# Kernel tuning notes

Hardware: AMD Instinct MI355X
Metric: run time of the kernel (lower is better)

Reference implementation:

```python
import jax, jax.numpy as jnp
import numpy as np

NUM_TIMESTEPS = 8  # num_timesteps default of CSSMDeiT3Block
LN_EPS = 1e-6      # flax nn.LayerNorm default


def _layernorm(x, scale, bias):
    mu = jnp.mean(x, axis=-1, keepdims=True)
    var = jnp.mean(jnp.square(x - mu), axis=-1, keepdims=True)
    return (x - mu) * jax.lax.rsqrt(var + LN_EPS) * scale + bias


def setup_inputs() -> dict:
    key = jax.random.key(0)
    ks = jax.random.split(key, 8)
    B, H, W, C = 32, 14, 14, 768
    HID = 4 * C
    s = lambda fan: np.float32(1.0 / np.sqrt(fan))
    return {
        "x": jax.random.normal(ks[0], (B, H, W, C), jnp.float32),
        # norm1
        "ln1_scale": jnp.ones((C,), jnp.float32),
        "ln1_bias": jnp.zeros((C,), jnp.float32),
        # GatedCSSM (opponent, concat_xy=True, sigmoid gate)
        "W_in": jax.random.normal(ks[1], (C, C), jnp.float32) * s(C),
        "b_in": jnp.zeros((C,), jnp.float32),
        "W_gate": jax.random.normal(ks[2], (2 * C, C), jnp.float32) * s(2 * C),
        "b_gate": jnp.zeros((C,), jnp.float32),
        "a_decay": jax.random.uniform(ks[3], (C,), jnp.float32, 0.5, 0.99),
        "b_rot": jax.random.normal(ks[4], (C,), jnp.float32) * 0.1,
        "W_out": jax.random.normal(ks[5], (C, C), jnp.float32) * s(C),
        "b_out": jnp.zeros((C,), jnp.float32),
        # layer scales (init_values = 1e-6)
        "gamma1": jnp.full((C,), 1e-6, jnp.float32),
        # norm2 + MLP
        "ln2_scale": jnp.ones((C,), jnp.float32),
        "ln2_bias": jnp.zeros((C,), jnp.float32),
        "W1": jax.random.normal(ks[6], (C, HID), jnp.float32) * s(C),
        "b1": jnp.zeros((HID,), jnp.float32),
        "W2": jax.random.normal(ks[7], (HID, C), jnp.float32) * s(HID),
        "b2": jnp.zeros((C,), jnp.float32),
        "gamma2": jnp.full((C,), 1e-6, jnp.float32),
    }


def reference(x, ln1_scale, ln1_bias, W_in, b_in, W_gate, b_gate, a_decay,
              b_rot, W_out, b_out, gamma1, ln2_scale, ln2_bias,
              W1, b1, W2, b2, gamma2):
    # ---- branch 1: pre-norm -> GatedCSSM (temporal recurrence) -> layerscale -> residual
    residual = x
    xn = _layernorm(x, ln1_scale, ln1_bias)
    # input is repeated over T timesteps, so project once and reuse
    u = xn @ W_in + b_in                       # (B,H,W,C)
    z0 = jnp.zeros_like(u)

    def step(carry, _):
        hx, hy = carry
        # concat_xy=True: gate computed from both opponent states
        g = jax.nn.sigmoid(jnp.concatenate([hx, hy], axis=-1) @ W_gate + b_gate)
        # opponent (rotation/decay) state-space update, gated
        hx_n = g * (a_decay * hx - b_rot * hy) + u
        hy_n = g * (b_rot * hx + a_decay * hy)
        return (hx_n, hy_n), None

    (hx, _hy), _ = jax.lax.scan(step, (z0, z0), None, length=NUM_TIMESTEPS)
    y = hx @ W_out + b_out                     # last-timestep readout (B,H,W,C)
    x = residual + y * gamma1                  # DropPath is identity (rate 0, deterministic)

    # ---- branch 2: pre-norm -> MLP(gelu) -> layerscale -> residual
    residual = x
    xn = _layernorm(x, ln2_scale, ln2_bias)
    h = jax.nn.gelu(xn @ W1 + b1)
    m = h @ W2 + b2
    return residual + m * gamma2
```

## Files before the change

kernel.cpp:

```cpp
#include <hip/hip_runtime.h>
#include <math.h>

typedef __bf16 bf16x8 __attribute__((ext_vector_type(8)));
typedef float  f32x4  __attribute__((ext_vector_type(4)));

#define NROWS 6272
#define CDIM  768
#define HIDD  3072

#define EPI_BIAS 0
#define EPI_GELU 2
#define EPI_RES  3

__device__ __forceinline__ void gload16(const void* g, void* l) {
    __builtin_amdgcn_global_load_lds(
        (const __attribute__((address_space(1))) void*)(uintptr_t)g,
        (__attribute__((address_space(3))) void*)(uintptr_t)l,
        16, 0, 0);
}

__device__ __forceinline__ void xcd_swz(int& m, int& n) {
    const int gx = gridDim.x;
    const int nwg = gx * gridDim.y;
    const int orig = blockIdx.x + gx * blockIdx.y;
    const int q = nwg >> 3, r = nwg & 7;
    const int xcd = orig & 7, loc = orig >> 3;
    const int wg = (xcd < r ? xcd * (q + 1) : r * (q + 1) + (xcd - r) * q) + loc;
    m = wg / gx;
    n = wg % gx;
}

template <int BM, int BN>
__device__ __forceinline__ void gemm_core(const __bf16* __restrict__ A, int lda,
                                          const __bf16* __restrict__ BT, int K,
                                          int m0, int n0,
                                          __bf16* As, __bf16* Bs,
                                          f32x4 acc[BM / 32][BN / 32]) {
    constexpr int RF = BM / 32;
    constexpr int CF = BN / 32;
    const int t  = threadIdx.x;
    const int w  = t >> 6;
    const int l  = t & 63;
    const int wm = w >> 1, wn = w & 1;
    const int rsub = t >> 2;
    const int ke   = (t & 3) * 8;
    const int fr = l & 15;
    const int kq = (l >> 4) * 8;

    const __bf16* gA = A  + (size_t)(m0 + rsub) * lda + ke;
    const __bf16* gB = BT + (size_t)(n0 + rsub) * K   + ke;
    __bf16* lA = &As[w * 512];
    __bf16* lB = &Bs[w * 512];

    for (int k0 = 0; k0 < K; k0 += 32) {
        __syncthreads();
        #pragma unroll
        for (int h = 0; h < BM / 64; ++h)
            gload16(gA + (size_t)(h * 64) * lda + k0, lA + h * 2048);
        #pragma unroll
        for (int h = 0; h < BN / 64; ++h)
            gload16(gB + (size_t)(h * 64) * K + k0, lB + h * 2048);
        __syncthreads();

        bf16x8 av[RF], bv[CF];
        #pragma unroll
        for (int i = 0; i < RF; ++i)
            av[i] = *(const bf16x8*)&As[(wm * (BM / 2) + i * 16 + fr) * 32 + kq];
        #pragma unroll
        for (int j = 0; j < CF; ++j)
            bv[j] = *(const bf16x8*)&Bs[(wn * (BN / 2) + j * 16 + fr) * 32 + kq];
        #pragma unroll
        for (int i = 0; i < RF; ++i)
            #pragma unroll
            for (int j = 0; j < CF; ++j)
                acc[i][j] = __builtin_amdgcn_mfma_f32_16x16x32_bf16(av[i], bv[j], acc[i][j], 0, 0, 0);
    }
}

__global__ __launch_bounds__(256) void transpose_all(const float* __restrict__ W_in,
                                                     const float* __restrict__ W_gate,
                                                     const float* __restrict__ W_out,
                                                     const float* __restrict__ W1,
                                                     const float* __restrict__ W2,
                                                     __bf16* __restrict__ WT_in,
                                                     __bf16* __restrict__ WT_gate,
                                                     __bf16* __restrict__ WT_out,
                                                     __bf16* __restrict__ WT1,
                                                     __bf16* __restrict__ WT2) {
    const int bid = blockIdx.x;
    const float* W; __bf16* WT; int K, N, gx, local;
    if (bid < 576)        { W = W_in;   WT = WT_in;   K = 768;  N = 768;  gx = 24; local = bid; }
    else if (bid < 1728)  { W = W_gate; WT = WT_gate; K = 1536; N = 768;  gx = 24; local = bid - 576; }
    else if (bid < 2304)  { W = W_out;  WT = WT_out;  K = 768;  N = 768;  gx = 24; local = bid - 1728; }
    else if (bid < 4608)  { W = W1;     WT = WT1;     K = 768;  N = 3072; gx = 96; local = bid - 2304; }
    else                  { W = W2;     WT = WT2;     K = 3072; N = 768;  gx = 24; local = bid - 4608; }
    const int nb = (local % gx) * 32;
    const int kb = (local / gx) * 32;

    __shared__ float tile[32][33];
    const int tx = threadIdx.x, ty = threadIdx.y;
    #pragma unroll
    for (int r = 0; r < 4; ++r)
        tile[ty + r * 8][tx] = W[(size_t)(kb + ty + r * 8) * N + nb + tx];
    __syncthreads();
    #pragma unroll
    for (int r = 0; r < 4; ++r)
        WT[(size_t)(nb + ty + r * 8) * K + kb + tx] = (__bf16)tile[tx][ty + r * 8];
}

__global__ __launch_bounds__(256) void ln_kernel(const float* __restrict__ x,
                                                 const float* __restrict__ sc,
                                                 const float* __restrict__ bi,
                                                 __bf16* __restrict__ o) {
    const int row = blockIdx.x;
    const float* xr = x + (size_t)row * CDIM;
    __bf16* orow = o + (size_t)row * CDIM;
    const int t = threadIdx.x;

    float v0 = xr[t], v1 = xr[t + 256], v2 = xr[t + 512];
    float s = v0 + v1 + v2;

    __shared__ float sm[8];
    #pragma unroll
    for (int off = 32; off > 0; off >>= 1) s += __shfl_xor(s, off);
    const int wid = t >> 6, lane = t & 63;
    if (lane == 0) sm[wid] = s;
    __syncthreads();
    const float mu = (sm[0] + sm[1] + sm[2] + sm[3]) * (1.0f / 768.0f);

    const float d0 = v0 - mu, d1 = v1 - mu, d2 = v2 - mu;
    float s2 = d0 * d0 + d1 * d1 + d2 * d2;
    #pragma unroll
    for (int off = 32; off > 0; off >>= 1) s2 += __shfl_xor(s2, off);
    if (lane == 0) sm[4 + wid] = s2;
    __syncthreads();
    const float var = (sm[4] + sm[5] + sm[6] + sm[7]) * (1.0f / 768.0f);
    const float r = rsqrtf(var + 1e-6f);

    orow[t]       = (__bf16)(d0 * r * sc[t]       + bi[t]);
    orow[t + 256] = (__bf16)(d1 * r * sc[t + 256] + bi[t + 256]);
    orow[t + 512] = (__bf16)(d2 * r * sc[t + 512] + bi[t + 512]);
}

template <int EPI, int BM, int BN>
__global__ __launch_bounds__(256) void mm_bf16(const __bf16* __restrict__ A, int lda,
                                               const __bf16* __restrict__ BT,
                                               const float* __restrict__ bias,
                                               const float* __restrict__ gamma,
                                               const float* __restrict__ res, int ldr,
                                               void* __restrict__ outv, int ldo,
                                               int K) {
    constexpr int RF = BM / 32;
    constexpr int CF = BN / 32;
    __shared__ __bf16 As[BM * 32];
    __shared__ __bf16 Bs[BN * 32];
    int mb, nb;
    xcd_swz(mb, nb);
    const int m0 = mb * BM, n0 = nb * BN;

    f32x4 acc[RF][CF];
    #pragma unroll
    for (int i = 0; i < RF; ++i)
        #pragma unroll
        for (int j = 0; j < CF; ++j)
            acc[i][j] = f32x4{0.f, 0.f, 0.f, 0.f};

    gemm_core<BM, BN>(A, lda, BT, K, m0, n0, As, Bs, acc);

    const int l = threadIdx.x & 63;
    const int w = threadIdx.x >> 6;
    const int wm = w >> 1, wn = w & 1;
    const int fr = l & 15;
    const int row0 = m0 + wm * (BM / 2);
    const int col0 = n0 + wn * (BN / 2);
    #pragma unroll
    for (int i = 0; i < RF; ++i) {
        #pragma unroll
        for (int j = 0; j < CF; ++j) {
            const int col = col0 + j * 16 + fr;
            const float bsv = bias[col];
            #pragma unroll
            for (int r = 0; r < 4; ++r) {
                const int row = row0 + i * 16 + (l >> 4) * 4 + r;
                float z = acc[i][j][r] + bsv;
                if (EPI == EPI_BIAS) {
                    ((__bf16*)outv)[(size_t)row * ldo + col] = (__bf16)z;
                } else if (EPI == EPI_GELU) {
                    const float z3 = z * z * z;
                    z = 0.5f * z * (1.0f + tanhf(0.7978845608028654f * (z + 0.044715f * z3)));
                    ((__bf16*)outv)[(size_t)row * ldo + col] = (__bf16)z;
                } else {
                    const float zz = res[(size_t)row * ldr + col] + z * gamma[col];
                    ((float*)outv)[(size_t)row * ldo + col] = zz;
                }
            }
        }
    }
}

template <bool LAST>
__global__ __launch_bounds__(256) void gate_step(const __bf16* __restrict__ hxy_cur,
                                                 const __bf16* __restrict__ WT_gate,
                                                 const float* __restrict__ b_gate,
                                                 const __bf16* __restrict__ u,
                                                 const float* __restrict__ ad,
                                                 const float* __restrict__ br,
                                                 __bf16* __restrict__ hxy_next) {
    constexpr int BM = 64, BN = 64;
    __shared__ __bf16 As[BM * 32];
    __shared__ __bf16 Bs[BN * 32];
    int mb, nb;
    xcd_swz(mb, nb);
    const int m0 = mb * BM, n0 = nb * BN;

    f32x4 acc[2][2];
    #pragma unroll
    for (int i = 0; i < 2; ++i)
        #pragma unroll
        for (int j = 0; j < 2; ++j)
            acc[i][j] = f32x4{0.f, 0.f, 0.f, 0.f};

    gemm_core<BM, BN>(hxy_cur, 1536, WT_gate, 1536, m0, n0, As, Bs, acc);

    const int l = threadIdx.x & 63;
    const int w = threadIdx.x >> 6;
    const int wm = w >> 1, wn = w & 1;
    const int fr = l & 15;
    const int row0 = m0 + wm * 32;
    const int col0 = n0 + wn * 32;
    #pragma unroll
    for (int i = 0; i < 2; ++i) {
        #pragma unroll
        for (int j = 0; j < 2; ++j) {
            const int col = col0 + j * 16 + fr;
            const float bg = b_gate[col];
            const float av = ad[col];
            const float bv = br[col];
            #pragma unroll
            for (int r = 0; r < 4; ++r) {
                const int row = row0 + i * 16 + (l >> 4) * 4 + r;
                float z = acc[i][j][r] + bg;
                z = 1.0f / (1.0f + __expf(-z));
                const size_t base = (size_t)row * 1536 + col;
                const float hx = (float)hxy_cur[base];
                const float hy = (float)hxy_cur[base + 768];
                const float uf = (float)u[(size_t)row * 768 + col];
                hxy_next[base] = (__bf16)(z * (av * hx - bv * hy) + uf);
                if (!LAST)
                    hxy_next[base + 768] = (__bf16)(z * (bv * hx + av * hy));
            }
        }
    }
}

__global__ __launch_bounds__(256) void init_state(const __bf16* __restrict__ u,
                                                  __bf16* __restrict__ hxy) {
    const int i = blockIdx.x * 256 + threadIdx.x;
    const int row = i / 96, c8 = i % 96;
    const bf16x8 uv = *(const bf16x8*)&u[(size_t)i * 8];
    *(bf16x8*)&hxy[(size_t)row * 1536 + c8 * 8] = uv;
    *(uint4*)&hxy[(size_t)row * 1536 + 768 + c8 * 8] = make_uint4(0u, 0u, 0u, 0u);
}

extern "C" void kernel_launch(void* const* d_in, const int* in_sizes, int n_in,
                              void* d_out, int out_size, void* d_ws, size_t ws_size,
                              hipStream_t stream) {
    (void)in_sizes; (void)n_in; (void)out_size;
    const float* x      = (const float*)d_in[0];
    const float* ln1_s  = (const float*)d_in[1];
    const float* ln1_b  = (const float*)d_in[2];
    const float* W_in   = (const float*)d_in[3];
    const float* b_in   = (const float*)d_in[4];
    const float* W_gate = (const float*)d_in[5];
    const float* b_gate = (const float*)d_in[6];
    const float* a_dec  = (const float*)d_in[7];
    const float* b_rot  = (const float*)d_in[8];
    const float* W_out  = (const float*)d_in[9];
    const float* b_out  = (const float*)d_in[10];
    const float* gamma1 = (const float*)d_in[11];
    const float* ln2_s  = (const float*)d_in[12];
    const float* ln2_b  = (const float*)d_in[13];
    const float* W1     = (const float*)d_in[14];
    const float* b1     = (const float*)d_in[15];
    const float* W2     = (const float*)d_in[16];
    const float* b2     = (const float*)d_in[17];
    const float* gamma2 = (const float*)d_in[18];
    float* out = (float*)d_out;

    if (ws_size < 92000000) return;
    char* w8 = (char*)d_ws;
    __bf16* WT_in   = (__bf16*)(w8);
    __bf16* WT_gate = (__bf16*)(w8 + 1179648);
    __bf16* WT_out  = (__bf16*)(w8 + 3538944);
    __bf16* WT1     = (__bf16*)(w8 + 4718592);
    __bf16* WT2     = (__bf16*)(w8 + 9437184);
    float*  x1      = (float*)(w8 + 14155776);
    __bf16* xn      = (__bf16*)(w8 + 33423360);
    __bf16* u       = (__bf16*)(w8 + 43057152);
    __bf16* hxy_a   = (__bf16*)(w8 + 52690944);
    __bf16* hxy_b   = (__bf16*)(w8 + 71958528);
    __bf16* h       = (__bf16*)(w8 + 52690944);

    transpose_all<<<6912, dim3(32, 8), 0, stream>>>(W_in, W_gate, W_out, W1, W2,
                                                    WT_in, WT_gate, WT_out, WT1, WT2);

    const dim3 gC(12, 98);
    const dim3 gH(24, 49);
    const int eb = 2352;

    ln_kernel<<<NROWS, 256, 0, stream>>>(x, ln1_s, ln1_b, xn);
    mm_bf16<EPI_BIAS, 64, 64><<<gC, 256, 0, stream>>>(xn, 768, WT_in, b_in,
                                                      nullptr, nullptr, 0, u, 768, 768);
    init_state<<<eb, 256, 0, stream>>>(u, hxy_a);
    __bf16* cur = hxy_a;
    __bf16* nxt = hxy_b;
    for (int ts = 1; ts < 8; ++ts) {
        if (ts == 7)
            gate_step<true><<<gC, 256, 0, stream>>>(cur, WT_gate, b_gate, u, a_dec, b_rot, nxt);
        else
            gate_step<false><<<gC, 256, 0, stream>>>(cur, WT_gate, b_gate, u, a_dec, b_rot, nxt);
        __bf16* tmp = cur; cur = nxt; nxt = tmp;
    }
    mm_bf16<EPI_RES, 64, 64><<<gC, 256, 0, stream>>>(cur, 1536, WT_out, b_out,
                                                     gamma1, x, 768, x1, 768, 768);
    ln_kernel<<<NROWS, 256, 0, stream>>>(x1, ln2_s, ln2_b, xn);
    mm_bf16<EPI_GELU, 128, 128><<<gH, 256, 0, stream>>>(xn, 768, WT1, b1,
                                                        nullptr, nullptr, 0, h, 3072, 768);
    mm_bf16<EPI_RES, 64, 64><<<gC, 256, 0, stream>>>(h, 3072, WT2, b2,
                                                     gamma2, x1, 768, out, 768, 3072);
}
```

Baseline: 584.3 us.

## Double-buffer GEMM LDS tiles, fuse state init into input projection, cheaper GELU

After: 569.4 us. 1.03x faster.

```diff
diff --git a/kernel.cpp b/kernel.cpp
--- a/kernel.cpp
+++ b/kernel.cpp
@@ -8,9 +8,9 @@
 #define CDIM  768
 #define HIDD  3072
 
-#define EPI_BIAS 0
-#define EPI_GELU 2
-#define EPI_RES  3
+#define EPI_UINIT 0
+#define EPI_GELU  2
+#define EPI_RES   3
 
 __device__ __forceinline__ void gload16(const void* g, void* l) {
     __builtin_amdgcn_global_load_lds(
@@ -38,6 +38,8 @@
                                           f32x4 acc[BM / 32][BN / 32]) {
     constexpr int RF = BM / 32;
     constexpr int CF = BN / 32;
+    constexpr int ASZ = BM * 32;
+    constexpr int BSZ = BN * 32;
     const int t  = threadIdx.x;
     const int w  = t >> 6;
     const int l  = t & 63;
@@ -49,26 +51,38 @@
 
     const __bf16* gA = A  + (size_t)(m0 + rsub) * lda + ke;
     const __bf16* gB = BT + (size_t)(n0 + rsub) * K   + ke;
-    __bf16* lA = &As[w * 512];
-    __bf16* lB = &Bs[w * 512];
-
-    for (int k0 = 0; k0 < K; k0 += 32) {
+
+    #pragma unroll
+    for (int h = 0; h < BM / 64; ++h)
+        gload16(gA + (size_t)(h * 64) * lda, As + w * 512 + h * 2048);
+    #pragma unroll
+    for (int h = 0; h < BN / 64; ++h)
+        gload16(gB + (size_t)(h * 64) * K, Bs + w * 512 + h * 2048);
+
+    const int NT = K >> 5;
+    #pragma unroll 2
+    for (int kt = 0; kt < NT; ++kt) {
+        const int cur = kt & 1;
         __syncthreads();
-        #pragma unroll
-        for (int h = 0; h < BM / 64; ++h)
-            gload16(gA + (size_t)(h * 64) * lda + k0, lA + h * 2048);
-        #pragma unroll
-        for (int h = 0; h < BN / 64; ++h)
-            gload16(gB + (size_t)(h * 64) * K + k0, lB + h * 2048);
-        __syncthreads();
-
+        if (kt + 1 < NT) {
+            const int k0 = (kt + 1) * 32;
+            const int nb = cur ^ 1;
+            #pragma unroll
+            for (int h = 0; h < BM / 64; ++h)
+                gload16(gA + (size_t)(h * 64) * lda + k0, As + nb * ASZ + w * 512 + h * 2048);
+            #pragma unroll
+            for (int h = 0; h < BN / 64; ++h)
+                gload16(gB + (size_t)(h * 64) * K + k0, Bs + nb * BSZ + w * 512 + h * 2048);
+        }
+        const __bf16* cA = As + cur * ASZ;
+        const __bf16* cB = Bs + cur * BSZ;
         bf16x8 av[RF], bv[CF];
         #pragma unroll
         for (int i = 0; i < RF; ++i)
-            av[i] = *(const bf16x8*)&As[(wm * (BM / 2) + i * 16 + fr) * 32 + kq];
+            av[i] = *(const bf16x8*)&cA[(wm * (BM / 2) + i * 16 + fr) * 32 + kq];
         #pragma unroll
         for (int j = 0; j < CF; ++j)
-            bv[j] = *(const bf16x8*)&Bs[(wn * (BN / 2) + j * 16 + fr) * 32 + kq];
+            bv[j] = *(const bf16x8*)&cB[(wn * (BN / 2) + j * 16 + fr) * 32 + kq];
         #pragma unroll
         for (int i = 0; i < RF; ++i)
             #pragma unroll
@@ -149,11 +163,11 @@
                                                const float* __restrict__ gamma,
                                                const float* __restrict__ res, int ldr,
                                                void* __restrict__ outv, int ldo,
-                                               int K) {
+                                               int K, __bf16* __restrict__ hxy0) {
     constexpr int RF = BM / 32;
     constexpr int CF = BN / 32;
-    __shared__ __bf16 As[BM * 32];
-    __shared__ __bf16 Bs[BN * 32];
+    __shared__ __bf16 As[2 * BM * 32];
+    __shared__ __bf16 Bs[2 * BN * 32];
     int mb, nb;
     xcd_swz(mb, nb);
     const int m0 = mb * BM, n0 = nb * BN;
@@ -183,12 +197,14 @@
             for (int r = 0; r < 4; ++r) {
                 const int row = row0 + i * 16 + (l >> 4) * 4 + r;
                 float z = acc[i][j][r] + bsv;
-                if (EPI == EPI_BIAS) {
+                if (EPI == EPI_UINIT) {
                     ((__bf16*)outv)[(size_t)row * ldo + col] = (__bf16)z;
+                    hxy0[(size_t)row * 1536 + col] = (__bf16)z;
+                    hxy0[(size_t)row * 1536 + 768 + col] = (__bf16)0.f;
                 } else if (EPI == EPI_GELU) {
-                    const float z3 = z * z * z;
-                    z = 0.5f * z * (1.0f + tanhf(0.7978845608028654f * (z + 0.044715f * z3)));
-                    ((__bf16*)outv)[(size_t)row * ldo + col] = (__bf16)z;
+                    const float v = 1.5957691216f * z * (1.0f + 0.044715f * z * z);
+                    const float sg = 1.0f / (1.0f + __expf(-v));
+                    ((__bf16*)outv)[(size_t)row * ldo + col] = (__bf16)(z * sg);
                 } else {
                     const float zz = res[(size_t)row * ldr + col] + z * gamma[col];
                     ((float*)outv)[(size_t)row * ldo + col] = zz;
@@ -207,8 +223,8 @@
                                                  const float* __restrict__ br,
                                                  __bf16* __restrict__ hxy_next) {
     constexpr int BM = 64, BN = 64;
-    __shared__ __bf16 As[BM * 32];
-    __shared__ __bf16 Bs[BN * 32];
+    __shared__ __bf16 As[2 * BM * 32];
+    __shared__ __bf16 Bs[2 * BN * 32];
     int mb, nb;
     xcd_swz(mb, nb);
     const int m0 = mb * BM, n0 = nb * BN;
@@ -251,15 +267,6 @@
             }
         }
     }
-}
-
-__global__ __launch_bounds__(256) void init_state(const __bf16* __restrict__ u,
-                                                  __bf16* __restrict__ hxy) {
-    const int i = blockIdx.x * 256 + threadIdx.x;
-    const int row = i / 96, c8 = i % 96;
-    const bf16x8 uv = *(const bf16x8*)&u[(size_t)i * 8];
-    *(bf16x8*)&hxy[(size_t)row * 1536 + c8 * 8] = uv;
-    *(uint4*)&hxy[(size_t)row * 1536 + 768 + c8 * 8] = make_uint4(0u, 0u, 0u, 0u);
 }
 
 extern "C" void kernel_launch(void* const* d_in, const int* in_sizes, int n_in,
@@ -306,12 +313,10 @@
 
     const dim3 gC(12, 98);
     const dim3 gH(24, 49);
-    const int eb = 2352;
 
     ln_kernel<<<NROWS, 256, 0, stream>>>(x, ln1_s, ln1_b, xn);
-    mm_bf16<EPI_BIAS, 64, 64><<<gC, 256, 0, stream>>>(xn, 768, WT_in, b_in,
-                                                      nullptr, nullptr, 0, u, 768, 768);
-    init_state<<<eb, 256, 0, stream>>>(u, hxy_a);
+    mm_bf16<EPI_UINIT, 64, 64><<<gC, 256, 0, stream>>>(xn, 768, WT_in, b_in,
+                                                       nullptr, nullptr, 0, u, 768, 768, hxy_a);
     __bf16* cur = hxy_a;
     __bf16* nxt = hxy_b;
     for (int ts = 1; ts < 8; ++ts) {
@@ -322,10 +327,10 @@
         __bf16* tmp = cur; cur = nxt; nxt = tmp;
     }
     mm_bf16<EPI_RES, 64, 64><<<gC, 256, 0, stream>>>(cur, 1536, WT_out, b_out,
-                                                     gamma1, x, 768, x1, 768, 768);
+                                                     gamma1, x, 768, x1, 768, 768, nullptr);
     ln_kernel<<<NROWS, 256, 0, stream>>>(x1, ln2_s, ln2_b, xn);
     mm_bf16<EPI_GELU, 128, 128><<<gH, 256, 0, stream>>>(xn, 768, WT1, b1,
-                                                        nullptr, nullptr, 0, h, 3072, 768);
+                                                        nullptr, nullptr, 0, h, 3072, 768, nullptr);
     mm_bf16<EPI_RES, 64, 64><<<gC, 256, 0, stream>>>(h, 3072, WT2, b2,
-                                                     gamma2, x1, 768, out, 768, 3072);
-}
+                                                     gamma2, x1, 768, out, 768, 3072, nullptr);
+}
```
